# Kernel optimization log

Measured on AMD Instinct MI355X. Metric: run time of the kernel, lower is better.

The kernel has to match this reference:

```python
import jax, jax.numpy as jnp
import numpy as np


def setup_inputs() -> dict:
    key = jax.random.key(0)
    k1, k2 = jax.random.split(key)
    N, H, W = 8, 64, 128
    flow = jax.random.normal(k1, (N, 2, H, W), dtype=jnp.float32)
    mask = jax.random.normal(k2, (N, 9 * 8 * 8, H, W), dtype=jnp.float32)
    return {"flow": flow, "mask": mask}


def reference(flow, mask):
    # flow: [N, 2, H, W], mask: [N, 576, H, W] -> up_flow: [N, 2, 8H, 8W]
    N, C, H, W = flow.shape  # C == 2
    m = mask.reshape(N, 9, 8, 8, H, W)  # (torch view had a leading 1-dim; broadcast instead)
    m = jax.nn.softmax(m, axis=1)  # softmax over the 9 neighbor weights

    # F.unfold(8*flow, [3,3], padding=1): 3x3 neighborhoods, row-major kernel order
    f = 8.0 * flow
    fp = jnp.pad(f, ((0, 0), (0, 0), (1, 1), (1, 1)))
    # patches: [N, 2, 9, H, W], k = di*3 + dj matches unfold's ordering per channel
    patches = jnp.stack(
        [fp[:, :, di:di + H, dj:dj + W] for di in range(3) for dj in range(3)],
        axis=2,
    )

    # convex combination: sum over the 9 neighbors -> [N, 2, 8, 8, H, W]
    up = jnp.einsum("nkabhw,nckhw->ncabhw", m, patches)
    # permute (0,1,4,2,5,3): [N, 2, H, 8, W, 8] then merge -> [N, 2, 8H, 8W]
    up = jnp.transpose(up, (0, 1, 4, 2, 5, 3))
    return up.reshape(N, C, 8 * H, 8 * W)
```

## Files before the change

kernel.cpp:

```cpp
#include <hip/hip_runtime.h>


#define N_ 8
#define H_ 64
#define W_ 128
#define HW_ (H_ * W_)

__global__ __launch_bounds__(128) void flow_up_kernel(
    const float* __restrict__ flow,
    const float* __restrict__ mask,
    float* __restrict__ out)
{
    const int bid = blockIdx.x;
    const int a = bid & 7;
    const int h = (bid >> 3) & (H_ - 1);
    const int n = bid >> 9;
    const int w = threadIdx.x;

    float p[2][9];
#pragma unroll
    for (int c = 0; c < 2; ++c) {
        const float* fbase = flow + (long)(n * 2 + c) * HW_;
#pragma unroll
        for (int di = 0; di < 3; ++di) {
            const int hh = h - 1 + di;
            const bool hin = (hh >= 0) && (hh < H_);
#pragma unroll
            for (int dj = 0; dj < 3; ++dj) {
                const int ww = w - 1 + dj;
                const bool in = hin && (ww >= 0) && (ww < W_);
                p[c][di * 3 + dj] = in ? 8.0f * fbase[hh * W_ + ww] : 0.0f;
            }
        }
    }

    const long mbase = ((long)n * 576 * HW_) + (long)h * W_ + w;
    const int qa = a * 8;

    float acc0[8], acc1[8];
#pragma unroll
    for (int b = 0; b < 8; ++b) {
        float e[9];
        float s = 0.0f;
#pragma unroll
        for (int k = 0; k < 9; ++k) {
            const int q = k * 64 + qa + b;
            const float m = mask[mbase + (long)q * HW_];
            e[k] = __expf(m);
            s += e[k];
        }
        const float inv = 1.0f / s;
        float o0 = 0.0f, o1 = 0.0f;
#pragma unroll
        for (int k = 0; k < 9; ++k) {
            o0 += e[k] * p[0][k];
            o1 += e[k] * p[1][k];
        }
        acc0[b] = o0 * inv;
        acc1[b] = o1 * inv;
    }

    const int y = h * 8 + a;
    float4* o0 = (float4*)(out + ((long)(n * 2 + 0) * (8 * H_) + y) * (8 * W_) + 8 * w);
    float4* o1 = (float4*)(out + ((long)(n * 2 + 1) * (8 * H_) + y) * (8 * W_) + 8 * w);
    o0[0] = make_float4(acc0[0], acc0[1], acc0[2], acc0[3]);
    o0[1] = make_float4(acc0[4], acc0[5], acc0[6], acc0[7]);
    o1[0] = make_float4(acc1[0], acc1[1], acc1[2], acc1[3]);
    o1[1] = make_float4(acc1[4], acc1[5], acc1[6], acc1[7]);
}

extern "C" void kernel_launch(void* const* d_in, const int* in_sizes, int n_in,
                              void* d_out, int out_size, void* d_ws, size_t ws_size,
                              hipStream_t stream) {
    const float* flow = (const float*)d_in[0];
    const float* mask = (const float*)d_in[1];
    float* out = (float*)d_out;

    const int grid = N_ * H_ * 8;
    flow_up_kernel<<<grid, 128, 0, stream>>>(flow, mask, out);
}
```

Baseline: 228.6 us.

## Clamp flow loads, fuse softmax accumulation, use fast reciprocal and 32-bit indexing

The flow neighbourhood loads now use clamped indices with a scale factor instead of conditional loads, which removes branches around memory accesses. Exponent summation and the weighted flow accumulation are fused into one loop, and the division is replaced with the hardware reciprocal. Indexing switches from 64-bit to 32-bit arithmetic and launch bounds add a minimum occupancy hint. The kernel is memory-bound on the mask reads, so these instruction-level savings may matter little, and the fast reciprocal slightly reduces precision.

```diff
diff --git a/kernel.cpp b/kernel.cpp
--- a/kernel.cpp
+++ b/kernel.cpp
@@ -6,7 +6,7 @@
 #define W_ 128
 #define HW_ (H_ * W_)
 
-__global__ __launch_bounds__(128) void flow_up_kernel(
+__global__ __launch_bounds__(128, 4) void flow_up_kernel(
     const float* __restrict__ flow,
     const float* __restrict__ mask,
     float* __restrict__ out)
@@ -17,56 +17,50 @@
     const int n = bid >> 9;
     const int w = threadIdx.x;
 
-    float p[2][9];
+    float p0[9], p1[9];
+    const float* __restrict__ f0 = flow + (n * 2 + 0) * HW_;
+    const float* __restrict__ f1 = flow + (n * 2 + 1) * HW_;
 #pragma unroll
-    for (int c = 0; c < 2; ++c) {
-        const float* fbase = flow + (long)(n * 2 + c) * HW_;
+    for (int di = 0; di < 3; ++di) {
+        const int hr = h - 1 + di;
+        const int hc = min(max(hr, 0), H_ - 1);
+        const bool hin = (hr >= 0) && (hr < H_);
 #pragma unroll
-        for (int di = 0; di < 3; ++di) {
-            const int hh = h - 1 + di;
-            const bool hin = (hh >= 0) && (hh < H_);
-#pragma unroll
-            for (int dj = 0; dj < 3; ++dj) {
-                const int ww = w - 1 + dj;
-                const bool in = hin && (ww >= 0) && (ww < W_);
-                p[c][di * 3 + dj] = in ? 8.0f * fbase[hh * W_ + ww] : 0.0f;
-            }
+        for (int dj = 0; dj < 3; ++dj) {
+            const int wr = w - 1 + dj;
+            const int wc = min(max(wr, 0), W_ - 1);
+            const float sc = (hin && wr >= 0 && wr < W_) ? 8.0f : 0.0f;
+            const int o = hc * W_ + wc;
+            p0[di * 3 + dj] = f0[o] * sc;
+            p1[di * 3 + dj] = f1[o] * sc;
         }
     }
 
-    const long mbase = ((long)n * 576 * HW_) + (long)h * W_ + w;
-    const int qa = a * 8;
+    const float* __restrict__ mp = mask + (n * 576 + a * 8) * HW_ + h * W_ + w;
 
     float acc0[8], acc1[8];
 #pragma unroll
     for (int b = 0; b < 8; ++b) {
-        float e[9];
-        float s = 0.0f;
+        float s = 0.0f, o0 = 0.0f, o1 = 0.0f;
 #pragma unroll
         for (int k = 0; k < 9; ++k) {
-            const int q = k * 64 + qa + b;
-            const float m = mask[mbase + (long)q * HW_];
-            e[k] = __expf(m);
-            s += e[k];
+            const float e = __expf(mp[(k * 64 + b) * HW_]);
+            s  += e;
+            o0 += e * p0[k];
+            o1 += e * p1[k];
         }
-        const float inv = 1.0f / s;
-        float o0 = 0.0f, o1 = 0.0f;
-#pragma unroll
-        for (int k = 0; k < 9; ++k) {
-            o0 += e[k] * p[0][k];
-            o1 += e[k] * p[1][k];
-        }
+        const float inv = __builtin_amdgcn_rcpf(s);
         acc0[b] = o0 * inv;
         acc1[b] = o1 * inv;
     }
 
     const int y = h * 8 + a;
-    float4* o0 = (float4*)(out + ((long)(n * 2 + 0) * (8 * H_) + y) * (8 * W_) + 8 * w);
-    float4* o1 = (float4*)(out + ((long)(n * 2 + 1) * (8 * H_) + y) * (8 * W_) + 8 * w);
-    o0[0] = make_float4(acc0[0], acc0[1], acc0[2], acc0[3]);
-    o0[1] = make_float4(acc0[4], acc0[5], acc0[6], acc0[7]);
-    o1[0] = make_float4(acc1[0], acc1[1], acc1[2], acc1[3]);
-    o1[1] = make_float4(acc1[4], acc1[5], acc1[6], acc1[7]);
+    float4* __restrict__ q0 = (float4*)(out + ((n * 2 + 0) * (8 * H_) + y) * (8 * W_) + 8 * w);
+    float4* __restrict__ q1 = (float4*)(out + ((n * 2 + 1) * (8 * H_) + y) * (8 * W_) + 8 * w);
+    q0[0] = make_float4(acc0[0], acc0[1], acc0[2], acc0[3]);
+    q0[1] = make_float4(acc0[4], acc0[5], acc0[6], acc0[7]);
+    q1[0] = make_float4(acc1[0], acc1[1], acc1[2], acc1[3]);
+    q1[1] = make_float4(acc1[4], acc1[5], acc1[6], acc1[7]);
 }
 
 extern "C" void kernel_launch(void* const* d_in, const int* in_sizes, int n_in,
```

Result: no change. 224.5 us (-1.8%).
